# Optimization experiments

Hardware: AMD Instinct MI355X
Metric: run time of the kernel (lower is better)

The kernel has to match this reference:

```python
import jax, jax.numpy as jnp
import numpy as np

EPS = 1e-5
# NOTE: TransmorpherLayer2d passes (dim_head, num_heads) into TiedAxialSelfAttention2d(num_heads, dim_head),
# so with init dim_head=64, num_heads=8 the attention effectively uses H=64 heads of C=8 channels each.
H = 64
C = 8


def _ln_ch(x, w, b):
    # AxialLayerNorm over channel dim (dim=1) of [B, D, S, L]
    m = x.mean(axis=1, keepdims=True)
    v = x.var(axis=1, keepdims=True)
    return (x - m) * jax.lax.rsqrt(v + EPS) * w[None, :, None, None] + b[None, :, None, None]


def _conv1x1(x, W, b):
    # Conv2d kernel_size=1: pointwise channel mix. W: [out, in], x: [B, in, S, L]
    return jnp.einsum('od,bdsl->bosl', W, x) + b[None, :, None, None]


def setup_inputs() -> dict:
    key = jax.random.key(0)
    ks = jax.random.split(key, 8)
    B, D, S, L, F = 1, 512, 64, 256, 2048
    g = lambda k, shape: jax.random.normal(k, shape, jnp.float32) * 0.02
    return {
        'x': jax.random.normal(ks[0], (B, D, S, L), jnp.float32),
        'w_row': g(ks[1], (3 * D, D)), 'b_row': jnp.zeros((3 * D,), jnp.float32),
        'w_col': g(ks[2], (3 * D, D)), 'b_col': jnp.zeros((3 * D,), jnp.float32),
        'w_an1': jnp.ones((D,), jnp.float32), 'b_an1': jnp.zeros((D,), jnp.float32),
        'w_an2': jnp.ones((D,), jnp.float32), 'b_an2': jnp.zeros((D,), jnp.float32),
        'w_ff1': g(ks[3], (F, D)), 'b_ff1': jnp.zeros((F,), jnp.float32),
        'w_ff2': g(ks[4], (D, F)), 'b_ff2': jnp.zeros((D,), jnp.float32),
        'w_ln1': jnp.ones((D,), jnp.float32), 'b_ln1': jnp.zeros((D,), jnp.float32),
        'w_ln2': jnp.ones((D,), jnp.float32), 'b_ln2': jnp.zeros((D,), jnp.float32),
    }


def _forward(x, w_row, b_row, w_col, b_col, w_an1, b_an1, w_an2, b_an2,
             w_ff1, b_ff1, w_ff2, b_ff2, w_ln1, b_ln1, w_ln2, b_ln2):
    B, D, S, L = x.shape
    # ---- tied row attention (attention tied across the S axis; no 1/sqrt scaling in source) ----
    qkv = _conv1x1(x, w_row, b_row)
    q, k, v = [t.reshape(B, H, C, S, L) for t in jnp.split(qkv, 3, axis=1)]
    row_attn = jax.nn.softmax(jnp.einsum('bhcsi,bhcsj->bhij', q, k), axis=-1)  # [B,H,L,L]
    row_out = jnp.einsum('bhij,bhdsj->bhdsi', row_attn, v).reshape(B, D, S, L)
    out = _ln_ch(x + row_out, w_an1, b_an1)
    # ---- column attention (softmax over key index j = dim -2) ----
    qkv = _conv1x1(out, w_col, b_col)
    q, k, v = [t.reshape(B, H, C, S, L) for t in jnp.split(qkv, 3, axis=1)]
    col_attn = jax.nn.softmax(jnp.einsum('bhcil,bhcjl->bhijl', q, k), axis=-2)  # [B,H,S,S,L]
    col_out = jnp.einsum('bhijl,bhdjl->bhdil', col_attn, v).reshape(B, D, S, L)
    attn_out = _ln_ch(out + col_out, w_an2, b_an2)
    # ---- layer body. Source bug kept faithfully: the attention residual `x + dropout1(out)`
    # is computed then discarded; norm1 is applied to the attention output only. ----
    h = _ln_ch(attn_out, w_ln1, b_ln1)
    ff = _conv1x1(jax.nn.relu(_conv1x1(h, w_ff1, b_ff1)), w_ff2, b_ff2)
    return _ln_ch(h + ff, w_ln2, b_ln2)


def reference(x, w_row, b_row, w_col, b_col, w_an1, b_an1, w_an2, b_an2,
              w_ff1, b_ff1, w_ff2, b_ff2, w_ln1, b_ln1, w_ln2, b_ln2):
    return _forward(x, w_row, b_row, w_col, b_col, w_an1, b_an1, w_an2, b_an2,
                    w_ff1, b_ff1, w_ff2, b_ff2, w_ln1, b_ln1, w_ln2, b_ln2)
```

## Files before the change

kernel.cpp:

```cpp
#include <hip/hip_runtime.h>
#include <hip/hip_bf16.h>

using s16x8 = __attribute__((ext_vector_type(8))) short;
using f32x4 = __attribute__((ext_vector_type(4))) float;
using u32x2 = __attribute__((ext_vector_type(2))) unsigned;

__device__ __forceinline__ ushort f2bf(float f) {
  union { float f; unsigned u; } v; v.f = f;
  unsigned r = v.u + 0x7fffu + ((v.u >> 16) & 1u);
  return (ushort)(r >> 16);
}
__device__ __forceinline__ float bf2f(ushort u) {
  return __uint_as_float(((unsigned)u) << 16);
}
__device__ __forceinline__ void gload16(const void* g, void* l) {
  __builtin_amdgcn_global_load_lds(
      (const __attribute__((address_space(1))) void*)g,
      (__attribute__((address_space(3))) void*)l, 16, 0, 0);
}

template<int AF, int BF, bool BIAS, bool RELU, int OUT, bool TRC>
__global__ __launch_bounds__(256, 3)
void gemm(void* __restrict__ Cv, const ushort* __restrict__ A,
          const ushort* __restrict__ B, const float* __restrict__ bias,
          int K, int lda, int ldb, int ldc, long sA, long sB, long sC)
{
  __shared__ ushort As[2][5120];
  __shared__ ushort Bs[2][5120];
  const int tid  = threadIdx.x;
  const int lane = tid & 63, wid = tid >> 6;
  const int gx = gridDim.x, gy = gridDim.y;
  const int lin = blockIdx.y * gx + blockIdx.x;
  int mb, nb;
  if ((gx & 7) == 0) {
    const int xcd = lin & 7, idx = lin >> 3, gxp = gx >> 3;
    nb = xcd * gxp + idx / gy;
    mb = idx % gy;
  } else {
    const int nwg = gx * gy;
    const int swz = ((nwg & 7) == 0) ? ((lin & 7) * (nwg >> 3) + (lin >> 3)) : lin;
    mb = swz / gx; nb = swz % gx;
  }
  const int m0 = mb * 128, n0 = nb * 128;
  A += (long)blockIdx.z * sA;
  B += (long)blockIdx.z * sB;

  const int wm = (wid >> 1) * 64, wn = (wid & 1) * 64;
  const int fr = lane & 15, kg = lane >> 4;

  f32x4 acc[4][4];
#pragma unroll
  for (int i = 0; i < 4; ++i)
#pragma unroll
    for (int j = 0; j < 4; ++j)
#pragma unroll
      for (int r = 0; r < 4; ++r) acc[i][j][r] = 0.f;

  auto stageT = [&](const ushort* __restrict__ G, int ld, int c0,
                    ushort* lds, int k0) {
#pragma unroll
    for (int c = 0; c < 2; ++c) {
      const int nb2 = wid * 2 + c;
      const ushort* gp = G + (long)(k0 + (lane >> 1)) * ld + c0 + nb2 * 16 + (lane & 1) * 8;
      gload16(gp, lds + nb2 * 512);
    }
  };
  auto loadN = [&](const ushort* __restrict__ G, int ld, int r0, int k0,
                   uint4& x, uint4& y) {
    const ushort* gp = G + (long)(r0 + (tid >> 1)) * ld + k0 + (tid & 1) * 8;
    x = *(const uint4*)gp;
    y = *(const uint4*)(gp + 16);
  };
  auto writeN = [&](ushort* lds, uint4 x, uint4 y) {
    ushort* p = lds + (tid >> 1) * 40 + (tid & 1) * 8;
    *(uint4*)p = x;
    *(uint4*)(p + 16) = y;
  };
  auto fragN = [&](const ushort* lds, int row) {
    union { s16x8 f; u32x2 h[2]; } u;
    const ushort* p = lds + row * 40 + kg * 4;
    u.h[0] = *(const u32x2*)p;
    u.h[1] = *(const u32x2*)(p + 16);
    return u.f;
  };
  auto fragT = [&](const ushort* lds, int rb) {
    union { s16x8 f; u32x2 h[2]; } u;
    unsigned base = (unsigned)(unsigned long long)(lds + rb * 512) + lane * 8;
    asm volatile("ds_read_b64_tr_b16 %0, %1" : "=v"(u.h[0]) : "v"(base));
    asm volatile("ds_read_b64_tr_b16 %0, %1 offset:512" : "=v"(u.h[1]) : "v"(base));
    return u.f;
  };

  const int NT = K >> 5;
  uint4 ax, ay, bx, by;

  if constexpr (AF == 0) { loadN(A, lda, m0, 0, ax, ay); writeN(As[0], ax, ay); }
  else                   { stageT(A, lda, m0, As[0], 0); }
  if constexpr (BF == 0) { loadN(B, ldb, n0, 0, bx, by); writeN(Bs[0], bx, by); }
  else                   { stageT(B, ldb, n0, Bs[0], 0); }
  __syncthreads();

  for (int t = 0; t < NT; ++t) {
    const int cur = t & 1, nxt = cur ^ 1;
    const bool pre = (t + 1) < NT;
    if (pre) {
      if constexpr (AF == 0) loadN(A, lda, m0, (t + 1) << 5, ax, ay);
      else                   stageT(A, lda, m0, As[nxt], (t + 1) << 5);
      if constexpr (BF == 0) loadN(B, ldb, n0, (t + 1) << 5, bx, by);
      else                   stageT(B, ldb, n0, Bs[nxt], (t + 1) << 5);
    }
    s16x8 af[4], bv[4];
#pragma unroll
    for (int m = 0; m < 4; ++m) {
      if constexpr (AF == 0) af[m] = fragN(As[cur], wm + m * 16 + fr);
      else                   af[m] = fragT(As[cur], (wm >> 4) + m);
    }
#pragma unroll
    for (int n = 0; n < 4; ++n) {
      if constexpr (BF == 0) bv[n] = fragN(Bs[cur], wn + n * 16 + fr);
      else                   bv[n] = fragT(Bs[cur], (wn >> 4) + n);
    }
    if constexpr (AF == 1 || BF == 1) {
      asm volatile("s_waitcnt lgkmcnt(0)");
      __builtin_amdgcn_sched_barrier(0);
    }
    __builtin_amdgcn_s_setprio(1);
#pragma unroll
    for (int m = 0; m < 4; ++m)
#pragma unroll
      for (int n = 0; n < 4; ++n)
        acc[m][n] = __builtin_amdgcn_mfma_f32_16x16x32_bf16(af[m], bv[n], acc[m][n], 0, 0, 0);
    __builtin_amdgcn_s_setprio(0);
    if (pre) {
      if constexpr (AF == 0) writeN(As[nxt], ax, ay);
      if constexpr (BF == 0) writeN(Bs[nxt], bx, by);
    }
    __syncthreads();
  }

#pragma unroll
  for (int m = 0; m < 4; ++m) {
    const int rowb = m0 + wm + m * 16 + kg * 4;
#pragma unroll
    for (int n = 0; n < 4; ++n) {
      const int col = n0 + wn + n * 16 + fr;
      f32x4 v = acc[m][n];
      if constexpr (BIAS) {
#pragma unroll
        for (int r = 0; r < 4; ++r) v[r] += bias[rowb + r];
      }
      if constexpr (RELU) {
#pragma unroll
        for (int r = 0; r < 4; ++r) v[r] = fmaxf(v[r], 0.f);
      }
      if constexpr (TRC) {
        float* C = (float*)Cv + (long)blockIdx.z * sC;
        float4 s; s.x = v[0]; s.y = v[1]; s.z = v[2]; s.w = v[3];
        *(float4*)(C + (long)col * ldc + rowb) = s;
      } else if constexpr (OUT == 0) {
        float* C = (float*)Cv + (long)blockIdx.z * sC;
#pragma unroll
        for (int r = 0; r < 4; ++r) C[(long)(rowb + r) * ldc + col] = v[r];
      } else {
        ushort* C = (ushort*)Cv + (long)blockIdx.z * sC;
#pragma unroll
        for (int r = 0; r < 4; ++r) C[(long)(rowb + r) * ldc + col] = f2bf(v[r]);
      }
    }
  }
}

__global__ __launch_bounds__(256)
void cvt_kernel(const float4* __restrict__ in, ushort4* __restrict__ out, int n4) {
  int i = blockIdx.x * 256 + threadIdx.x;
  if (i < n4) {
    float4 f = in[i];
    ushort4 u; u.x = f2bf(f.x); u.y = f2bf(f.y); u.z = f2bf(f.z); u.w = f2bf(f.w);
    out[i] = u;
  }
}

__global__ __launch_bounds__(256)
void softmax_kernel(const float* __restrict__ S, ushort* __restrict__ P) {
  const int row = blockIdx.x * 4 + (threadIdx.x >> 6);
  const int lane = threadIdx.x & 63;
  float4 v = *(const float4*)(S + (long)row * 256 + lane * 4);
  float mx = fmaxf(fmaxf(v.x, v.y), fmaxf(v.z, v.w));
#pragma unroll
  for (int off = 32; off; off >>= 1) mx = fmaxf(mx, __shfl_xor(mx, off));
  v.x = __expf(v.x - mx); v.y = __expf(v.y - mx);
  v.z = __expf(v.z - mx); v.w = __expf(v.w - mx);
  float s = v.x + v.y + v.z + v.w;
#pragma unroll
  for (int off = 32; off; off >>= 1) s += __shfl_xor(s, off);
  const float r = 1.f / s;
  ushort4 o;
  o.x = f2bf(v.x * r); o.y = f2bf(v.y * r); o.z = f2bf(v.z * r); o.w = f2bf(v.w * r);
  *(ushort4*)(P + (long)row * 256 + lane * 4) = o;
}

__global__ __launch_bounds__(256)
void colattn_kernel(const ushort* __restrict__ qkv, float* __restrict__ out) {
  __shared__ float q[4][8][64], kk[4][8][64], vv[4][8][64];
  const int lin = blockIdx.x;
  const int swz = (lin & 7) * 512 + (lin >> 3);
  const int h = swz >> 6;
  const int l0 = (swz & 63) * 4;
  const int tid = threadIdx.x;
  for (int i = tid; i < 1536; i += 256) {
    int m = i >> 9;
    int e = i & 511;
    int c = e >> 6, s = e & 63;
    ushort4 u = *(const ushort4*)(qkv + (long)(m * 512 + h * 8 + c) * 16384 + s * 256 + l0);
    float* dst = (m == 0) ? &q[0][0][0] : (m == 1) ? &kk[0][0][0] : &vv[0][0][0];
    dst[e] = bf2f(u.x); dst[512 + e] = bf2f(u.y);
    dst[1024 + e] = bf2f(u.z); dst[1536 + e] = bf2f(u.w);
  }
  __syncthreads();
  const int li = tid >> 6, lane = tid & 63;
  float qi[8];
#pragma unroll
  for (int c = 0; c < 8; ++c) qi[c] = q[li][c][lane];
  float sc[64];
#pragma unroll
  for (int j = 0; j < 64; ++j) {
    float s = 0.f;
#pragma unroll
    for (int c = 0; c < 8; ++c) s += qi[c] * kk[li][c][j];
    sc[j] = s;
  }
  float mx = sc[0];
#pragma unroll
  for (int j = 1; j < 64; ++j) mx = fmaxf(mx, sc[j]);
  float sum = 0.f;
#pragma unroll
  for (int j = 0; j < 64; ++j) { sc[j] = __expf(sc[j] - mx); sum += sc[j]; }
  const float rs = 1.f / sum;
  float o[8];
#pragma unroll
  for (int c = 0; c < 8; ++c) o[c] = 0.f;
#pragma unroll
  for (int j = 0; j < 64; ++j)
#pragma unroll
    for (int c = 0; c < 8; ++c) o[c] += sc[j] * vv[li][c][j];
#pragma unroll
  for (int c = 0; c < 8; ++c) q[li][c][lane] = o[c] * rs;
  __syncthreads();
  for (int i = tid; i < 512; i += 256) {
    int c = i >> 6, s = i & 63;
    float4 f; f.x = q[0][c][s]; f.y = q[1][c][s]; f.z = q[2][c][s]; f.w = q[3][c][s];
    *(float4*)(out + (long)(h * 8 + c) * 16384 + s * 256 + l0) = f;
  }
}

template<bool RES, bool BFO>
__global__ __launch_bounds__(1024)
void ln_kernel(float* __restrict__ out, ushort* __restrict__ bfo,
               const float* __restrict__ a, const float* __restrict__ b,
               const float* __restrict__ w, const float* __restrict__ bias) {
  __shared__ float red[2][16][64];
  const int lane = threadIdx.x & 63, seg = threadIdx.x >> 6;
  const long n = (long)blockIdx.x * 64 + lane;
  const int d0 = seg * 32;
  float v[32];
  float s1 = 0.f, s2 = 0.f;
#pragma unroll
  for (int i = 0; i < 32; ++i) {
    float t = a[(long)(d0 + i) * 16384 + n];
    if constexpr (RES) t += b[(long)(d0 + i) * 16384 + n];
    v[i] = t; s1 += t; s2 += t * t;
  }
  red[0][seg][lane] = s1; red[1][seg][lane] = s2;
  __syncthreads();
  s1 = 0.f; s2 = 0.f;
#pragma unroll
  for (int s = 0; s < 16; ++s) { s1 += red[0][s][lane]; s2 += red[1][s][lane]; }
  const float mean = s1 * (1.f / 512.f);
  const float var = s2 * (1.f / 512.f) - mean * mean;
  const float rstd = rsqrtf(var + 1e-5f);
#pragma unroll
  for (int i = 0; i < 32; ++i) {
    float o = (v[i] - mean) * rstd * w[d0 + i] + bias[d0 + i];
    out[(long)(d0 + i) * 16384 + n] = o;
    if constexpr (BFO) bfo[(long)(d0 + i) * 16384 + n] = f2bf(o);
  }
}

__global__ __launch_bounds__(1024)
void ln_fuse_kernel(float* __restrict__ out, ushort* __restrict__ bfo,
                    const float* __restrict__ a, const float* __restrict__ b,
                    const float* __restrict__ w1, const float* __restrict__ b1,
                    const float* __restrict__ w2, const float* __restrict__ b2) {
  __shared__ float red[2][16][64];
  const int lane = threadIdx.x & 63, seg = threadIdx.x >> 6;
  const long n = (long)blockIdx.x * 64 + lane;
  const int d0 = seg * 32;
  float v[32];
  float s1 = 0.f, s2 = 0.f;
#pragma unroll
  for (int i = 0; i < 32; ++i) {
    float t = a[(long)(d0 + i) * 16384 + n] + b[(long)(d0 + i) * 16384 + n];
    v[i] = t; s1 += t; s2 += t * t;
  }
  red[0][seg][lane] = s1; red[1][seg][lane] = s2;
  __syncthreads();
  s1 = 0.f; s2 = 0.f;
#pragma unroll
  for (int s = 0; s < 16; ++s) { s1 += red[0][s][lane]; s2 += red[1][s][lane]; }
  float mean = s1 * (1.f / 512.f);
  float var = s2 * (1.f / 512.f) - mean * mean;
  float rstd = rsqrtf(var + 1e-5f);
  __syncthreads();
  s1 = 0.f; s2 = 0.f;
#pragma unroll
  for (int i = 0; i < 32; ++i) {
    float y = (v[i] - mean) * rstd * w1[d0 + i] + b1[d0 + i];
    v[i] = y; s1 += y; s2 += y * y;
  }
  red[0][seg][lane] = s1; red[1][seg][lane] = s2;
  __syncthreads();
  s1 = 0.f; s2 = 0.f;
#pragma unroll
  for (int s = 0; s < 16; ++s) { s1 += red[0][s][lane]; s2 += red[1][s][lane]; }
  mean = s1 * (1.f / 512.f);
  var = s2 * (1.f / 512.f) - mean * mean;
  rstd = rsqrtf(var + 1e-5f);
#pragma unroll
  for (int i = 0; i < 32; ++i) {
    float o = (v[i] - mean) * rstd * w2[d0 + i] + b2[d0 + i];
    out[(long)(d0 + i) * 16384 + n] = o;
    bfo[(long)(d0 + i) * 16384 + n] = f2bf(o);
  }
}

extern "C" void kernel_launch(void* const* d_in, const int* in_sizes, int n_in,
                              void* d_out, int out_size, void* d_ws, size_t ws_size,
                              hipStream_t stream) {
  const float* x     = (const float*)d_in[0];
  const float* w_row = (const float*)d_in[1];
  const float* b_row = (const float*)d_in[2];
  const float* w_col = (const float*)d_in[3];
  const float* b_col = (const float*)d_in[4];
  const float* w_an1 = (const float*)d_in[5];
  const float* b_an1 = (const float*)d_in[6];
  const float* w_an2 = (const float*)d_in[7];
  const float* b_an2 = (const float*)d_in[8];
  const float* w_ff1 = (const float*)d_in[9];
  const float* b_ff1 = (const float*)d_in[10];
  const float* w_ff2 = (const float*)d_in[11];
  const float* b_ff2 = (const float*)d_in[12];
  const float* w_ln1 = (const float*)d_in[13];
  const float* b_ln1 = (const float*)d_in[14];
  const float* w_ln2 = (const float*)d_in[15];
  const float* b_ln2 = (const float*)d_in[16];
  float* outp = (float*)d_out;

  char* Wb = (char*)d_ws;
  ushort* big   = (ushort*)Wb;
  float*  sc    = (float*)(Wb + (size_t)1536 * 16384 * 2);
  float*  bufA  = (float*)(Wb + 67108864ull);
  float*  bufB  = (float*)(Wb + 100663296ull);
  ushort* P     = (ushort*)(Wb + 134217728ull);
  ushort* actbf = (ushort*)(Wb + 167772160ull);
  ushort* xbf   = actbf;
  ushort* wrowb = (ushort*)(Wb + 184549376ull);
  ushort* wcolb = wrowb + 786432;
  ushort* wff1b = wcolb + 786432;
  ushort* wff2b = wff1b + 1048576;

  const dim3 blk(256);
  const long HQ = 131072;
  const long HS = 65536;

  cvt_kernel<<<8192, blk, 0, stream>>>((const float4*)x, (ushort4*)xbf, 2097152);
  cvt_kernel<<<768,  blk, 0, stream>>>((const float4*)w_row, (ushort4*)wrowb, 196608);
  cvt_kernel<<<768,  blk, 0, stream>>>((const float4*)w_col, (ushort4*)wcolb, 196608);
  cvt_kernel<<<1024, blk, 0, stream>>>((const float4*)w_ff1, (ushort4*)wff1b, 262144);
  cvt_kernel<<<1024, blk, 0, stream>>>((const float4*)w_ff2, (ushort4*)wff2b, 262144);

  gemm<0,1,true,false,1,false><<<dim3(128, 12, 1), blk, 0, stream>>>(
      big, wrowb, xbf, b_row, 512, 512, 16384, 16384, 0, 0, 0);
  gemm<1,1,false,false,0,false><<<dim3(2, 2, 64), blk, 0, stream>>>(
      sc, big, big + (long)512 * 16384, nullptr, 512, 256, 256, 256, HQ, HQ, HS);
  softmax_kernel<<<4096, blk, 0, stream>>>(sc, P);
  gemm<0,0,false,false,0,true><<<dim3(4, 2, 64), blk, 0, stream>>>(
      bufA, P, big + (long)1024 * 16384, nullptr, 256, 256, 256, 256, HS, HQ, HQ);
  ln_kernel<true, true><<<256, dim3(1024), 0, stream>>>(bufB, actbf, x, bufA, w_an1, b_an1);
  gemm<0,1,true,false,1,false><<<dim3(128, 12, 1), blk, 0, stream>>>(
      big, wcolb, actbf, b_col, 512, 512, 16384, 16384, 0, 0, 0);
  colattn_kernel<<<4096, blk, 0, stream>>>(big, bufA);
  ln_fuse_kernel<<<256, dim3(1024), 0, stream>>>(bufB, actbf, bufB, bufA,
                                                 w_an2, b_an2, w_ln1, b_ln1);
  gemm<0,1,true,true,1,false><<<dim3(128, 16, 1), blk, 0, stream>>>(
      big, wff1b, actbf, b_ff1, 512, 512, 16384, 16384, 0, 0, 0);
  gemm<0,1,true,false,0,false><<<dim3(128, 4, 1), blk, 0, stream>>>(
      bufA, wff2b, big, b_ff2, 2048, 2048, 16384, 16384, 0, 0, 0);
  ln_kernel<true, false><<<256, dim3(1024), 0, stream>>>(outp, nullptr, bufB, bufA, w_ln2, b_ln2);
}
```

Baseline: 477.8 us.

## Store intermediate activations in bf16 and vectorize column-attention LDS reads

All fp32 intermediate activations (row-attention output, layernorm outputs, column-attention output, FF2 output) are now kept in bf16. Layernorm kernels read bf16 inputs and no longer write a separate fp32 copy, and the workspace is reorganised to hold these bf16 buffers. This roughly halves the memory traffic of the bandwidth-bound layernorm and epilogue stages, at the cost of extra rounding error on residual paths. The column-attention inner loops also switch to float4 shared-memory reads with FMAs.

```diff
diff --git a/kernel.cpp b/kernel.cpp
--- a/kernel.cpp
+++ b/kernel.cpp
@@ -154,9 +154,15 @@
         for (int r = 0; r < 4; ++r) v[r] = fmaxf(v[r], 0.f);
       }
       if constexpr (TRC) {
-        float* C = (float*)Cv + (long)blockIdx.z * sC;
-        float4 s; s.x = v[0]; s.y = v[1]; s.z = v[2]; s.w = v[3];
-        *(float4*)(C + (long)col * ldc + rowb) = s;
+        if constexpr (OUT == 0) {
+          float* C = (float*)Cv + (long)blockIdx.z * sC;
+          float4 s; s.x = v[0]; s.y = v[1]; s.z = v[2]; s.w = v[3];
+          *(float4*)(C + (long)col * ldc + rowb) = s;
+        } else {
+          ushort* C = (ushort*)Cv + (long)blockIdx.z * sC;
+          ushort4 s; s.x = f2bf(v[0]); s.y = f2bf(v[1]); s.z = f2bf(v[2]); s.w = f2bf(v[3]);
+          *(ushort4*)(C + (long)col * ldc + rowb) = s;
+        }
       } else if constexpr (OUT == 0) {
         float* C = (float*)Cv + (long)blockIdx.z * sC;
 #pragma unroll
@@ -200,7 +206,7 @@
 }
 
 __global__ __launch_bounds__(256)
-void colattn_kernel(const ushort* __restrict__ qkv, float* __restrict__ out) {
+void colattn_kernel(const ushort* __restrict__ qkv, ushort* __restrict__ out) {
   __shared__ float q[4][8][64], kk[4][8][64], vv[4][8][64];
   const int lin = blockIdx.x;
   const int swz = (lin & 7) * 512 + (lin >> 3);
@@ -223,11 +229,16 @@
   for (int c = 0; c < 8; ++c) qi[c] = q[li][c][lane];
   float sc[64];
 #pragma unroll
-  for (int j = 0; j < 64; ++j) {
-    float s = 0.f;
-#pragma unroll
-    for (int c = 0; c < 8; ++c) s += qi[c] * kk[li][c][j];
-    sc[j] = s;
+  for (int j4 = 0; j4 < 16; ++j4) {
+    float ax = 0.f, ay = 0.f, az = 0.f, aw = 0.f;
+#pragma unroll
+    for (int c = 0; c < 8; ++c) {
+      float4 k4 = *(const float4*)&kk[li][c][j4 * 4];
+      ax = fmaf(qi[c], k4.x, ax); ay = fmaf(qi[c], k4.y, ay);
+      az = fmaf(qi[c], k4.z, az); aw = fmaf(qi[c], k4.w, aw);
+    }
+    sc[j4 * 4 + 0] = ax; sc[j4 * 4 + 1] = ay;
+    sc[j4 * 4 + 2] = az; sc[j4 * 4 + 3] = aw;
   }
   float mx = sc[0];
 #pragma unroll
@@ -240,24 +251,32 @@
 #pragma unroll
   for (int c = 0; c < 8; ++c) o[c] = 0.f;
 #pragma unroll
-  for (int j = 0; j < 64; ++j)
-#pragma unroll
-    for (int c = 0; c < 8; ++c) o[c] += sc[j] * vv[li][c][j];
+  for (int j4 = 0; j4 < 16; ++j4) {
+    const float px = sc[j4 * 4 + 0], py = sc[j4 * 4 + 1];
+    const float pz = sc[j4 * 4 + 2], pw = sc[j4 * 4 + 3];
+#pragma unroll
+    for (int c = 0; c < 8; ++c) {
+      float4 v4 = *(const float4*)&vv[li][c][j4 * 4];
+      o[c] = fmaf(px, v4.x, fmaf(py, v4.y, fmaf(pz, v4.z, fmaf(pw, v4.w, o[c]))));
+    }
+  }
 #pragma unroll
   for (int c = 0; c < 8; ++c) q[li][c][lane] = o[c] * rs;
   __syncthreads();
   for (int i = tid; i < 512; i += 256) {
     int c = i >> 6, s = i & 63;
-    float4 f; f.x = q[0][c][s]; f.y = q[1][c][s]; f.z = q[2][c][s]; f.w = q[3][c][s];
-    *(float4*)(out + (long)(h * 8 + c) * 16384 + s * 256 + l0) = f;
-  }
-}
-
-template<bool RES, bool BFO>
+    ushort4 u;
+    u.x = f2bf(q[0][c][s]); u.y = f2bf(q[1][c][s]);
+    u.z = f2bf(q[2][c][s]); u.w = f2bf(q[3][c][s]);
+    *(ushort4*)(out + (long)(h * 8 + c) * 16384 + s * 256 + l0) = u;
+  }
+}
+
+template<bool RES, int OM>
 __global__ __launch_bounds__(1024)
-void ln_kernel(float* __restrict__ out, ushort* __restrict__ bfo,
-               const float* __restrict__ a, const float* __restrict__ b,
-               const float* __restrict__ w, const float* __restrict__ bias) {
+void ln_kernel(void* __restrict__ outv, const ushort* __restrict__ a,
+               const ushort* __restrict__ b, const float* __restrict__ w,
+               const float* __restrict__ bias) {
   __shared__ float red[2][16][64];
   const int lane = threadIdx.x & 63, seg = threadIdx.x >> 6;
   const long n = (long)blockIdx.x * 64 + lane;
@@ -266,8 +285,8 @@
   float s1 = 0.f, s2 = 0.f;
 #pragma unroll
   for (int i = 0; i < 32; ++i) {
-    float t = a[(long)(d0 + i) * 16384 + n];
-    if constexpr (RES) t += b[(long)(d0 + i) * 16384 + n];
+    float t = bf2f(a[(long)(d0 + i) * 16384 + n]);
+    if constexpr (RES) t += bf2f(b[(long)(d0 + i) * 16384 + n]);
     v[i] = t; s1 += t; s2 += t * t;
   }
   red[0][seg][lane] = s1; red[1][seg][lane] = s2;
@@ -281,14 +300,14 @@
 #pragma unroll
   for (int i = 0; i < 32; ++i) {
     float o = (v[i] - mean) * rstd * w[d0 + i] + bias[d0 + i];
-    out[(long)(d0 + i) * 16384 + n] = o;
-    if constexpr (BFO) bfo[(long)(d0 + i) * 16384 + n] = f2bf(o);
+    if constexpr (OM == 0) ((ushort*)outv)[(long)(d0 + i) * 16384 + n] = f2bf(o);
+    else                   ((float*)outv)[(long)(d0 + i) * 16384 + n] = o;
   }
 }
 
 __global__ __launch_bounds__(1024)
-void ln_fuse_kernel(float* __restrict__ out, ushort* __restrict__ bfo,
-                    const float* __restrict__ a, const float* __restrict__ b,
+void ln_fuse_kernel(ushort* __restrict__ out, const ushort* __restrict__ a,
+                    const ushort* __restrict__ b,
                     const float* __restrict__ w1, const float* __restrict__ b1,
                     const float* __restrict__ w2, const float* __restrict__ b2) {
   __shared__ float red[2][16][64];
@@ -299,7 +318,7 @@
   float s1 = 0.f, s2 = 0.f;
 #pragma unroll
   for (int i = 0; i < 32; ++i) {
-    float t = a[(long)(d0 + i) * 16384 + n] + b[(long)(d0 + i) * 16384 + n];
+    float t = bf2f(a[(long)(d0 + i) * 16384 + n]) + bf2f(b[(long)(d0 + i) * 16384 + n]);
     v[i] = t; s1 += t; s2 += t * t;
   }
   red[0][seg][lane] = s1; red[1][seg][lane] = s2;
@@ -328,8 +347,7 @@
 #pragma unroll
   for (int i = 0; i < 32; ++i) {
     float o = (v[i] - mean) * rstd * w2[d0 + i] + b2[d0 + i];
-    out[(long)(d0 + i) * 16384 + n] = o;
-    bfo[(long)(d0 + i) * 16384 + n] = f2bf(o);
+    out[(long)(d0 + i) * 16384 + n] = f2bf(o);
   }
 }
 
@@ -356,14 +374,16 @@
   float* outp = (float*)d_out;
 
   char* Wb = (char*)d_ws;
-  ushort* big   = (ushort*)Wb;
-  float*  sc    = (float*)(Wb + (size_t)1536 * 16384 * 2);
-  float*  bufA  = (float*)(Wb + 67108864ull);
-  float*  bufB  = (float*)(Wb + 100663296ull);
-  ushort* P     = (ushort*)(Wb + 134217728ull);
-  ushort* actbf = (ushort*)(Wb + 167772160ull);
-  ushort* xbf   = actbf;
-  ushort* wrowb = (ushort*)(Wb + 184549376ull);
+  ushort* big    = (ushort*)Wb;
+  float*  sc     = (float*)(Wb + 71303168ull);
+  ushort* colbf  = (ushort*)(Wb + 71303168ull);
+  ushort* P      = (ushort*)(Wb + 90177536ull);
+  ushort* xbf    = (ushort*)(Wb + 100663296ull);
+  ushort* ff2bf  = (ushort*)(Wb + 100663296ull);
+  ushort* rowbf  = (ushort*)(Wb + 118489088ull);
+  ushort* out1bf = (ushort*)(Wb + 136314880ull);
+  ushort* hbf    = (ushort*)(Wb + 154140672ull);
+  ushort* wrowb  = (ushort*)(Wb + 171966464ull);
   ushort* wcolb = wrowb + 786432;
   ushort* wff1b = wcolb + 786432;
   ushort* wff2b = wff1b + 1048576;
@@ -383,17 +403,17 @@
   gemm<1,1,false,false,0,false><<<dim3(2, 2, 64), blk, 0, stream>>>(
       sc, big, big + (long)512 * 16384, nullptr, 512, 256, 256, 256, HQ, HQ, HS);
   softmax_kernel<<<4096, blk, 0, stream>>>(sc, P);
-  gemm<0,0,false,false,0,true><<<dim3(4, 2, 64), blk, 0, stream>>>(
-      bufA, P, big + (long)1024 * 16384, nullptr, 256, 256, 256, 256, HS, HQ, HQ);
-  ln_kernel<true, true><<<256, dim3(1024), 0, stream>>>(bufB, actbf, x, bufA, w_an1, b_an1);
+  gemm<0,0,false,false,1,true><<<dim3(4, 2, 64), blk, 0, stream>>>(
+      rowbf, P, big + (long)1024 * 16384, nullptr, 256, 256, 256, 256, HS, HQ, HQ);
+  ln_kernel<true, 0><<<256, dim3(1024), 0, stream>>>(out1bf, xbf, rowbf, w_an1, b_an1);
   gemm<0,1,true,false,1,false><<<dim3(128, 12, 1), blk, 0, stream>>>(
-      big, wcolb, actbf, b_col, 512, 512, 16384, 16384, 0, 0, 0);
-  colattn_kernel<<<4096, blk, 0, stream>>>(big, bufA);
-  ln_fuse_kernel<<<256, dim3(1024), 0, stream>>>(bufB, actbf, bufB, bufA,
+      big, wcolb, out1bf, b_col, 512, 512, 16384, 16384, 0, 0, 0);
+  colattn_kernel<<<4096, blk, 0, stream>>>(big, colbf);
+  ln_fuse_kernel<<<256, dim3(1024), 0, stream>>>(hbf, out1bf, colbf,
                                                  w_an2, b_an2, w_ln1, b_ln1);
   gemm<0,1,true,true,1,false><<<dim3(128, 16, 1), blk, 0, stream>>>(
-      big, wff1b, actbf, b_ff1, 512, 512, 16384, 16384, 0, 0, 0);
-  gemm<0,1,true,false,0,false><<<dim3(128, 4, 1), blk, 0, stream>>>(
-      bufA, wff2b, big, b_ff2, 2048, 2048, 16384, 16384, 0, 0, 0);
-  ln_kernel<true, false><<<256, dim3(1024), 0, stream>>>(outp, nullptr, bufB, bufA, w_ln2, b_ln2);
-}
+      big, wff1b, hbf, b_ff1, 512, 512, 16384, 16384, 0, 0, 0);
+  gemm<0,1,true,false,1,false><<<dim3(128, 4, 1), blk, 0, stream>>>(
+      ff2bf, wff2b, big, b_ff2, 2048, 2048, 16384, 16384, 0, 0, 0);
+  ln_kernel<true, 1><<<256, dim3(1024), 0, stream>>>(outp, hbf, ff2bf, w_ln2, b_ln2);
+}
```

New measurement: 433.7 us. 9.2% less time.
